# Performance work log

Hardware: AMD Instinct MI355X
Metric: run time of the kernel (lower is better)

Reference implementation:

```python
import jax, jax.numpy as jnp
import numpy as np


def _run_lstm(x, W, U, b, mask=None):
    """Keras-style LSTM returning final hidden state.
    x: [N, T, D] float; W: [D, 4u]; U: [u, 4u]; b: [4u]; mask: [N, T] bool or None.
    Gate order i, f, g(c), o as in Keras. Masked steps carry state through.
    """
    N, T, D = x.shape
    units = U.shape[0]
    xt = jnp.transpose(x, (1, 0, 2))  # [T, N, D]
    if mask is not None:
        mt = jnp.transpose(mask, (1, 0))[:, :, None]  # [T, N, 1]
        xs = (xt, mt)
    else:
        xs = xt

    def step(carry, inp):
        h, c = carry
        if mask is not None:
            x_t, m = inp
        else:
            x_t = inp
        z = x_t @ W + h @ U + b  # [N, 4u]
        i, f, g, o = jnp.split(z, 4, axis=-1)
        i = jax.nn.sigmoid(i)
        f = jax.nn.sigmoid(f)
        g = jnp.tanh(g)
        o = jax.nn.sigmoid(o)
        c_new = f * c + i * g
        h_new = o * jnp.tanh(c_new)
        if mask is not None:
            h_new = jnp.where(m, h_new, h)
            c_new = jnp.where(m, c_new, c)
        return (h_new, c_new), None

    h0 = jnp.zeros((N, units), dtype=x.dtype)
    c0 = jnp.zeros((N, units), dtype=x.dtype)
    (hT, _), _ = jax.lax.scan(step, (h0, c0), xs)
    return hT


def setup_inputs() -> dict:
    key = jax.random.key(0)
    ks = jax.random.split(key, 10)
    B, T, S, D = 256, 256, 20, 1
    U1, U2 = 32, 24  # inner / outer LSTM units
    sc = 0.1
    x = jax.random.normal(ks[0], (B, T, S, D), dtype=jnp.float32)
    lengths = jax.random.randint(ks[1], (B,), 1, T + 1, dtype=jnp.int32)
    Wi = jax.random.normal(ks[2], (D, 4 * U1), dtype=jnp.float32) * sc
    Ui = jax.random.normal(ks[3], (U1, 4 * U1), dtype=jnp.float32) * sc
    bi = jnp.zeros((4 * U1,), dtype=jnp.float32)
    Wo = jax.random.normal(ks[4], (U1, 4 * U2), dtype=jnp.float32) * sc
    Uo = jax.random.normal(ks[5], (U2, 4 * U2), dtype=jnp.float32) * sc
    bo = jnp.zeros((4 * U2,), dtype=jnp.float32)
    Wd = jax.random.normal(ks[6], (U2, 1), dtype=jnp.float32) * sc
    bd = jnp.zeros((1,), dtype=jnp.float32)
    return {"x": x, "lengths": lengths, "Wi": Wi, "Ui": Ui, "bi": bi,
            "Wo": Wo, "Uo": Uo, "bo": bo, "Wd": Wd, "bd": bd}


def reference(x, lengths, Wi, Ui, bi, Wo, Uo, bo, Wd, bd):
    B, T, S, D = x.shape
    # TimeDistributed(LSTM(32)): run inner LSTM over each outer step (inference, dropout off)
    rows = x.reshape(B * T, S, D)
    h_inner = _run_lstm(rows, Wi, Ui, bi)          # [B*T, 32]
    feats = h_inner.reshape(B, T, -1)              # [B, T, 32]
    # Outer LSTM(24) with ragged-length mask (Keras mask semantics: carry state)
    mask = jnp.arange(T)[None, :] < lengths[:, None]  # [B, T]
    h_outer = _run_lstm(feats, Wo, Uo, bo, mask)   # [B, 24]
    # Dense sigmoid head
    return jax.nn.sigmoid(h_outer @ Wd + bd)       # [B, 1]
```

## Files before the change

### kernel.cpp

```cpp
#include <hip/hip_runtime.h>

#define B_  256
#define T_  256
#define S_  20
#define U1  32
#define G1  128
#define U2  24
#define G2  96
#define NT  16

typedef __attribute__((ext_vector_type(8))) short short8;
typedef __attribute__((ext_vector_type(4))) float f32x4;

__device__ __forceinline__ float sigmoidf_(float x) {
    return __builtin_amdgcn_rcpf(1.0f + __builtin_amdgcn_exp2f(x * -1.44269504f));
}
__device__ __forceinline__ float tanhf_fast(float x) {
    return 1.0f - 2.0f * __builtin_amdgcn_rcpf(1.0f + __builtin_amdgcn_exp2f(x * 2.88539008f));
}

__device__ __forceinline__ unsigned short f2bf(float a) {
    unsigned int u = __float_as_uint(a);
    u += 0x7FFFu + ((u >> 16) & 1u);
    return (unsigned short)(u >> 16);
}
__device__ __forceinline__ unsigned int pack2bf(float a, float b) {
    unsigned int ua = __float_as_uint(a); ua += 0x7FFFu + ((ua >> 16) & 1u);
    unsigned int ub = __float_as_uint(b); ub += 0x7FFFu + ((ub >> 16) & 1u);
    return (ua >> 16) | (ub & 0xFFFF0000u);
}
union frag_u { short8 v; unsigned int u[4]; };
union h2x  { unsigned int u32; _Float16 h[2]; };

__global__ __attribute__((amdgpu_flat_work_group_size(256, 256)))
__attribute__((amdgpu_waves_per_eu(1, 1)))
void fused_kernel(
    const float* __restrict__ x,
    const int*   __restrict__ lengths,
    const float* __restrict__ Wi,
    const float* __restrict__ Ui,
    const float* __restrict__ bi,
    const float* __restrict__ Wo,
    const float* __restrict__ Uo,
    const float* __restrict__ bo,
    const float* __restrict__ Wd,
    const float* __restrict__ bd,
    float* __restrict__ out)
{
    __shared__ __align__(16) _Float16      Pl[T_][G2];
    __shared__ __align__(16) unsigned short hbb[4][16][40];
    __shared__ unsigned int flags[NT];
    const int b    = blockIdx.x;
    const int len  = lengths[b];
    const int tid  = threadIdx.x;
    const int w    = __builtin_amdgcn_readfirstlane(tid >> 6);
    const int lane = tid & 63;
    const int q    = lane >> 4;
    const int n    = lane & 15;

    if (tid < NT) flags[tid] = 0;
    __syncthreads();

    frag_u Bui[8];
#pragma unroll
    for (int tt = 0; tt < 8; ++tt)
#pragma unroll
        for (int k2 = 0; k2 < 4; ++k2)
            Bui[tt].u[k2] = pack2bf(Ui[(8 * q + 2 * k2) * G1 + 16 * tt + n],
                                    Ui[(8 * q + 2 * k2 + 1) * G1 + 16 * tt + n]);
    frag_u Bwo[6];
#pragma unroll
    for (int tt = 0; tt < 6; ++tt)
#pragma unroll
        for (int k2 = 0; k2 < 4; ++k2)
            Bwo[tt].u[k2] = pack2bf(Wo[(8 * q + 2 * k2) * G2 + 16 * tt + n],
                                    Wo[(8 * q + 2 * k2 + 1) * G2 + 16 * tt + n]);
    float bi_l[8], Wi_l[8], bo_l[6];
#pragma unroll
    for (int tt = 0; tt < 8; ++tt) { bi_l[tt] = bi[16 * tt + n]; Wi_l[tt] = Wi[16 * tt + n]; }
#pragma unroll
    for (int tt = 0; tt < 6; ++tt) bo_l[tt] = bo[16 * tt + n];
    int pcol[6];
#pragma unroll
    for (int tt = 0; tt < 6; ++tt) {
        const int col = 16 * tt + n;
        const int g = col / 24;
        pcol[tt] = (col - 24 * g) * 4 + g;
    }

    const int ntl = (w == 0) ? 1 : 5;

#pragma unroll 1
    for (int i = 0; i < ntl; ++i) {
        const int tile = (w == 0) ? 0 : (w + 3 * i);
        const int wt0  = tile * 16;
        if (wt0 >= len) break;

        const float* xr = x + (size_t)(b * T_ + wt0 + 4 * q) * S_;
        float c[2][4];
#pragma unroll
        for (int uh = 0; uh < 2; ++uh)
#pragma unroll
            for (int r = 0; r < 4; ++r) c[uh][r] = 0.0f;

        float xc[4];
#pragma unroll
        for (int r = 0; r < 4; ++r) xc[r] = xr[r * S_];

        {
            f32x4 acc[8];
#pragma unroll
            for (int tt = 0; tt < 8; ++tt)
#pragma unroll
                for (int r = 0; r < 4; ++r)
                    acc[tt][r] = bi_l[tt] + xc[r] * Wi_l[tt];
#pragma unroll
            for (int uh = 0; uh < 2; ++uh)
#pragma unroll
                for (int r = 0; r < 4; ++r) {
                    const float iv = sigmoidf_(acc[0 + uh][r]);
                    const float fv = sigmoidf_(acc[2 + uh][r]);
                    const float gv = tanhf_fast(acc[4 + uh][r]);
                    const float ov = sigmoidf_(acc[6 + uh][r]);
                    c[uh][r] = fv * c[uh][r] + iv * gv;
                    hbb[w][4 * q + r][n + 16 * uh] = f2bf(ov * tanhf_fast(c[uh][r]));
                }
        }
#pragma unroll
        for (int r = 0; r < 4; ++r) xc[r] = xr[r * S_ + 1];

#pragma unroll 1
        for (int s = 1; s < S_; ++s) {
            const int sn = (s + 1 < S_) ? s + 1 : S_ - 1;
            float xnx[4];
#pragma unroll
            for (int r = 0; r < 4; ++r) xnx[r] = xr[r * S_ + sn];

            f32x4 acc[8];
#pragma unroll
            for (int tt = 0; tt < 8; ++tt)
#pragma unroll
                for (int r = 0; r < 4; ++r)
                    acc[tt][r] = bi_l[tt] + xc[r] * Wi_l[tt];

            const short8 A = *(const short8*)&hbb[w][n][8 * q];
#pragma unroll
            for (int tt = 0; tt < 8; ++tt)
                acc[tt] = __builtin_amdgcn_mfma_f32_16x16x32_bf16(A, Bui[tt].v, acc[tt], 0, 0, 0);

#pragma unroll
            for (int uh = 0; uh < 2; ++uh)
#pragma unroll
                for (int r = 0; r < 4; ++r) {
                    const float iv = sigmoidf_(acc[0 + uh][r]);
                    const float fv = sigmoidf_(acc[2 + uh][r]);
                    const float gv = tanhf_fast(acc[4 + uh][r]);
                    const float ov = sigmoidf_(acc[6 + uh][r]);
                    c[uh][r] = fv * c[uh][r] + iv * gv;
                    hbb[w][4 * q + r][n + 16 * uh] = f2bf(ov * tanhf_fast(c[uh][r]));
                }
#pragma unroll
            for (int r = 0; r < 4; ++r) xc[r] = xnx[r];
        }

        {
            const short8 A = *(const short8*)&hbb[w][n][8 * q];
            f32x4 accp[6];
#pragma unroll
            for (int tt = 0; tt < 6; ++tt) {
#pragma unroll
                for (int r = 0; r < 4; ++r) accp[tt][r] = bo_l[tt];
                accp[tt] = __builtin_amdgcn_mfma_f32_16x16x32_bf16(A, Bwo[tt].v, accp[tt], 0, 0, 0);
            }
#pragma unroll
            for (int r = 0; r < 4; ++r) {
                const int tr = wt0 + 4 * q + r;
#pragma unroll
                for (int tt = 0; tt < 6; ++tt)
                    Pl[tr][pcol[tt]] = (_Float16)accp[tt][r];
            }
        }
        __hip_atomic_store(&flags[tile], 1u, __ATOMIC_RELEASE, __HIP_MEMORY_SCOPE_WORKGROUP);
    }

    if (w != 0) return;

    const int half = lane >> 5;
    const int sub  = lane & 31;
    const int u    = (sub < U2) ? sub : U2 - 1;

    float wA[U2], wB[U2];
#pragma unroll
    for (int k = 0; k < U2; ++k) {
        wA[k] = Uo[k * G2 + (2 * half) * U2 + u];
        wB[k] = Uo[k * G2 + (2 * half + 1) * U2 + u];
    }

    auto ldrow = [&](int t) -> f32x4 {
        const uint2 raw = *reinterpret_cast<const uint2*>(&Pl[t][4 * u]);
        h2x a, c2; a.u32 = raw.x; c2.u32 = raw.y;
        f32x4 r;
        r[0] = (float)a.h[0];  r[1] = (float)a.h[1];
        r[2] = (float)c2.h[0]; r[3] = (float)c2.h[1];
        return r;
    };

    f32x4 cur = ldrow(0);
    float cu, hu;
    {
        const float ig = sigmoidf_(cur[0]);
        const float gg = tanhf_fast(cur[2]);
        const float og = sigmoidf_(cur[3]);
        cu = ig * gg;
        hu = og * tanhf_fast(cu);
    }
    int wtile = 0;
    f32x4 nxt = ldrow((1 < len) ? 1 : 0);

#pragma unroll 1
    for (int t = 1; t < len; ++t) {
        const int tn = (t + 1 < len) ? (t + 1) : (len - 1);
        const int ttile = tn >> 4;
        if (ttile != wtile) {
            while (__hip_atomic_load(&flags[ttile], __ATOMIC_ACQUIRE,
                                     __HIP_MEMORY_SCOPE_WORKGROUP) == 0u)
                __builtin_amdgcn_s_sleep(1);
            wtile = ttile;
        }
        const f32x4 pf = ldrow(tn);

        float hk[U2];
#pragma unroll
        for (int k = 0; k < U2; ++k)
            hk[k] = __int_as_float(__builtin_amdgcn_readlane(__float_as_int(hu), k));

        const float pA = half ? nxt[2] : nxt[0];
        const float pB = half ? nxt[3] : nxt[1];
        float a0 = pA, a1 = 0.0f, a2 = 0.0f, a3 = 0.0f;
        float b0 = pB, b1 = 0.0f, b2 = 0.0f, b3 = 0.0f;
#pragma unroll
        for (int k = 0; k < U2; k += 4) {
            a0 += hk[k]     * wA[k];     b0 += hk[k]     * wB[k];
            a1 += hk[k + 1] * wA[k + 1]; b1 += hk[k + 1] * wB[k + 1];
            a2 += hk[k + 2] * wA[k + 2]; b2 += hk[k + 2] * wB[k + 2];
            a3 += hk[k + 3] * wA[k + 3]; b3 += hk[k + 3] * wB[k + 3];
        }
        const float zA = (a0 + a1) + (a2 + a3);
        const float zB = (b0 + b1) + (b2 + b3);
        const float oA = __shfl_xor(zA, 32);
        const float oB = __shfl_xor(zB, 32);

        const float z_i = half ? oA : zA;
        const float z_f = half ? oB : zB;
        const float z_g = half ? zA : oA;
        const float z_o = half ? zB : oB;

        const float ig = sigmoidf_(z_i);
        const float fg = sigmoidf_(z_f);
        const float gg = tanhf_fast(z_g);
        const float og = sigmoidf_(z_o);
        cu = fg * cu + ig * gg;
        hu = og * tanhf_fast(cu);

        nxt = pf;
    }

    float acc = bd[0];
#pragma unroll
    for (int k = 0; k < U2; ++k)
        acc += __int_as_float(__builtin_amdgcn_readlane(__float_as_int(hu), k)) * Wd[k];
    if (lane == 0) out[b] = sigmoidf_(acc);
}

extern "C" void kernel_launch(void* const* d_in, const int* in_sizes, int n_in,
                              void* d_out, int out_size, void* d_ws, size_t ws_size,
                              hipStream_t stream) {
    const float* x       = (const float*)d_in[0];
    const int*   lengths = (const int*)  d_in[1];
    const float* Wi      = (const float*)d_in[2];
    const float* Ui      = (const float*)d_in[3];
    const float* bi      = (const float*)d_in[4];
    const float* Wo      = (const float*)d_in[5];
    const float* Uo      = (const float*)d_in[6];
    const float* bo      = (const float*)d_in[7];
    const float* Wd      = (const float*)d_in[8];
    const float* bd      = (const float*)d_in[9];
    float* out = (float*)d_out;

    fused_kernel<<<dim3(B_), dim3(256), 0, stream>>>(
        x, lengths, Wi, Ui, bi, Wo, Uo, bo, Wd, bd, out);
}
```

Before: 165.5 us.

## Compute all four outer-LSTM gates per lane with packed FMA, tile-split recurrence loop

The outer LSTM recurrence now has each of 24 lanes compute all four gates with packed two-wide FMAs. Previously the gate work was split across two wave halves and recombined with cross-half shuffles, which this removes. The loop is also restructured into per-tile inner loops, so the flag check moves out of the per-step path and happens only at tile boundaries. The cost is more FMAs per lane on the serial critical path, in exchange for dropping the two shuffles and the per-step tile branch.

```diff
diff --git a/kernel.cpp b/kernel.cpp
--- a/kernel.cpp
+++ b/kernel.cpp
@@ -11,6 +11,16 @@
 
 typedef __attribute__((ext_vector_type(8))) short short8;
 typedef __attribute__((ext_vector_type(4))) float f32x4;
+typedef __attribute__((ext_vector_type(2))) float f32x2;
+
+__device__ __forceinline__ f32x2 pkfma(f32x2 a, f32x2 b, f32x2 c) {
+#if __has_builtin(__builtin_elementwise_fma)
+    return __builtin_elementwise_fma(a, b, c);
+#else
+    f32x2 r; r[0] = __builtin_fmaf(a[0], b[0], c[0]); r[1] = __builtin_fmaf(a[1], b[1], c[1]);
+    return r;
+#endif
+}
 
 __device__ __forceinline__ float sigmoidf_(float x) {
     return __builtin_amdgcn_rcpf(1.0f + __builtin_amdgcn_exp2f(x * -1.44269504f));
@@ -89,7 +99,6 @@
     }
 
     const int ntl = (w == 0) ? 1 : 5;
-
 #pragma unroll 1
     for (int i = 0; i < ntl; ++i) {
         const int tile = (w == 0) ? 0 : (w + 3 * i);
@@ -185,15 +194,15 @@
 
     if (w != 0) return;
 
-    const int half = lane >> 5;
-    const int sub  = lane & 31;
-    const int u    = (sub < U2) ? sub : U2 - 1;
-
-    float wA[U2], wB[U2];
+    const int u = (lane < U2) ? lane : U2 - 1;
+
+    f32x2 wIF[U2], wGO[U2];
 #pragma unroll
     for (int k = 0; k < U2; ++k) {
-        wA[k] = Uo[k * G2 + (2 * half) * U2 + u];
-        wB[k] = Uo[k * G2 + (2 * half + 1) * U2 + u];
+        wIF[k][0] = Uo[k * G2 + 0 * U2 + u];
+        wIF[k][1] = Uo[k * G2 + 1 * U2 + u];
+        wGO[k][0] = Uo[k * G2 + 2 * U2 + u];
+        wGO[k][1] = Uo[k * G2 + 3 * U2 + u];
     }
 
     auto ldrow = [&](int t) -> f32x4 {
@@ -205,64 +214,85 @@
         return r;
     };
 
-    f32x4 cur = ldrow(0);
     float cu, hu;
     {
-        const float ig = sigmoidf_(cur[0]);
-        const float gg = tanhf_fast(cur[2]);
-        const float og = sigmoidf_(cur[3]);
+        const f32x4 r0 = ldrow(0);
+        const float ig = sigmoidf_(r0[0]);
+        const float gg = tanhf_fast(r0[2]);
+        const float og = sigmoidf_(r0[3]);
         cu = ig * gg;
         hu = og * tanhf_fast(cu);
     }
-    int wtile = 0;
+
+    int t = 1, tile = 0;
+    int tend = (16 < len) ? 16 : len;
     f32x4 nxt = ldrow((1 < len) ? 1 : 0);
 
 #pragma unroll 1
-    for (int t = 1; t < len; ++t) {
-        const int tn = (t + 1 < len) ? (t + 1) : (len - 1);
-        const int ttile = tn >> 4;
-        if (ttile != wtile) {
-            while (__hip_atomic_load(&flags[ttile], __ATOMIC_ACQUIRE,
+    while (t < len) {
+#pragma unroll 1
+        for (; t + 1 < tend; ++t) {
+            const f32x4 pf = ldrow(t + 1);
+
+            f32x2 zIF0 = { nxt[0], nxt[1] }, zIF1 = { 0.0f, 0.0f };
+            f32x2 zGO0 = { nxt[2], nxt[3] }, zGO1 = { 0.0f, 0.0f };
+#pragma unroll
+            for (int k = 0; k < U2; k += 2) {
+                const float h0 = __int_as_float(__builtin_amdgcn_readlane(__float_as_int(hu), k));
+                const float h1 = __int_as_float(__builtin_amdgcn_readlane(__float_as_int(hu), k + 1));
+                const f32x2 h02 = { h0, h0 }, h12 = { h1, h1 };
+                zIF0 = pkfma(wIF[k],     h02, zIF0);
+                zGO0 = pkfma(wGO[k],     h02, zGO0);
+                zIF1 = pkfma(wIF[k + 1], h12, zIF1);
+                zGO1 = pkfma(wGO[k + 1], h12, zGO1);
+            }
+            const f32x2 zIF = zIF0 + zIF1;
+            const f32x2 zGO = zGO0 + zGO1;
+
+            const float ig = sigmoidf_(zIF[0]);
+            const float fg = sigmoidf_(zIF[1]);
+            const float gg = tanhf_fast(zGO[0]);
+            const float og = sigmoidf_(zGO[1]);
+            cu = fg * cu + ig * gg;
+            hu = og * tanhf_fast(cu);
+            nxt = pf;
+        }
+
+        f32x4 pf = nxt;
+        const bool more = (tend < len);
+        if (more) {
+            ++tile;
+            while (__hip_atomic_load(&flags[tile], __ATOMIC_ACQUIRE,
                                      __HIP_MEMORY_SCOPE_WORKGROUP) == 0u)
                 __builtin_amdgcn_s_sleep(1);
-            wtile = ttile;
-        }
-        const f32x4 pf = ldrow(tn);
-
-        float hk[U2];
-#pragma unroll
-        for (int k = 0; k < U2; ++k)
-            hk[k] = __int_as_float(__builtin_amdgcn_readlane(__float_as_int(hu), k));
-
-        const float pA = half ? nxt[2] : nxt[0];
-        const float pB = half ? nxt[3] : nxt[1];
-        float a0 = pA, a1 = 0.0f, a2 = 0.0f, a3 = 0.0f;
-        float b0 = pB, b1 = 0.0f, b2 = 0.0f, b3 = 0.0f;
-#pragma unroll
-        for (int k = 0; k < U2; k += 4) {
-            a0 += hk[k]     * wA[k];     b0 += hk[k]     * wB[k];
-            a1 += hk[k + 1] * wA[k + 1]; b1 += hk[k + 1] * wB[k + 1];
-            a2 += hk[k + 2] * wA[k + 2]; b2 += hk[k + 2] * wB[k + 2];
-            a3 += hk[k + 3] * wA[k + 3]; b3 += hk[k + 3] * wB[k + 3];
-        }
-        const float zA = (a0 + a1) + (a2 + a3);
-        const float zB = (b0 + b1) + (b2 + b3);
-        const float oA = __shfl_xor(zA, 32);
-        const float oB = __shfl_xor(zB, 32);
-
-        const float z_i = half ? oA : zA;
-        const float z_f = half ? oB : zB;
-        const float z_g = half ? zA : oA;
-        const float z_o = half ? zB : oB;
-
-        const float ig = sigmoidf_(z_i);
-        const float fg = sigmoidf_(z_f);
-        const float gg = tanhf_fast(z_g);
-        const float og = sigmoidf_(z_o);
-        cu = fg * cu + ig * gg;
-        hu = og * tanhf_fast(cu);
-
+            pf = ldrow(tend);
+        }
+        {
+            f32x2 zIF0 = { nxt[0], nxt[1] }, zIF1 = { 0.0f, 0.0f };
+            f32x2 zGO0 = { nxt[2], nxt[3] }, zGO1 = { 0.0f, 0.0f };
+#pragma unroll
+            for (int k = 0; k < U2; k += 2) {
+                const float h0 = __int_as_float(__builtin_amdgcn_readlane(__float_as_int(hu), k));
+                const float h1 = __int_as_float(__builtin_amdgcn_readlane(__float_as_int(hu), k + 1));
+                const f32x2 h02 = { h0, h0 }, h12 = { h1, h1 };
+                zIF0 = pkfma(wIF[k],     h02, zIF0);
+                zGO0 = pkfma(wGO[k],     h02, zGO0);
+                zIF1 = pkfma(wIF[k + 1], h12, zIF1);
+                zGO1 = pkfma(wGO[k + 1], h12, zGO1);
+            }
+            const f32x2 zIF = zIF0 + zIF1;
+            const f32x2 zGO = zGO0 + zGO1;
+
+            const float ig = sigmoidf_(zIF[0]);
+            const float fg = sigmoidf_(zIF[1]);
+            const float gg = tanhf_fast(zGO[0]);
+            const float og = sigmoidf_(zGO[1]);
+            cu = fg * cu + ig * gg;
+            hu = og * tanhf_fast(cu);
+        }
+        ++t;
         nxt = pf;
+        tend = (tend + 16 < len) ? tend + 16 : len;
     }
 
     float acc = bd[0];
```

New measurement: 166.4 us. Within noise of the previous version (+0.5%).
